# Optimization experiments

Hardware: AMD Instinct MI355X
Metric: run time of the kernel (lower is better)

The kernel has to match this reference:

```python
import jax, jax.numpy as jnp
import numpy as np

VOCAB = 50257
D = 768      # d_model
E = 4        # n_experts
R = 32       # low-rank expert rank
B = 4        # batch
T = 512      # seq_len
LN_EPS = 1e-5


def setup_inputs() -> dict:
    key = jax.random.key(0)
    ks = jax.random.split(key, 8)
    n = lambda k, shape, scale: jax.random.normal(k, shape, dtype=jnp.float32) * scale
    return {
        "idx": jax.random.randint(ks[0], (B, T), 0, VOCAB),
        "W_emb": n(ks[1], (VOCAB, D), 0.02),            # tied embedding / lm head
        "G": n(ks[2], (E, D), 0.02),                     # expert gating signatures
        "W_in": n(ks[3], (E, D, R), 1.0 / np.sqrt(D)),   # per-expert input proj
        "W_rec": n(ks[4], (E, R, R), 1.0 / np.sqrt(R)),  # per-expert recurrent matrix
        "W_out": n(ks[5], (E, R, D), 1.0 / np.sqrt(R)),  # per-expert output proj
        "ln_gamma": jnp.ones((D,), dtype=jnp.float32),
        "ln_beta": jnp.zeros((D,), dtype=jnp.float32),
    }


def _layernorm(x, g, b):
    m = jnp.mean(x, axis=-1, keepdims=True)
    v = jnp.var(x, axis=-1, keepdims=True)
    return (x - m) * jax.lax.rsqrt(v + LN_EPS) * g + b


def reference(idx, W_emb, G, W_in, W_rec, W_out, ln_gamma, ln_beta):
    # idx: [B,T] int64 token ids
    x = W_emb[idx]                      # [B,T,D] embedding gather
    xT = jnp.swapaxes(x, 0, 1)          # [T,B,D] scan over time
    nE, nR = W_in.shape[0], W_in.shape[2]
    s0 = jnp.zeros((nE, idx.shape[0], nR), dtype=x.dtype)  # reset_state at t=0

    def step(states, x_t):
        # states: [E,B,R] per-expert recurrent state; x_t: [B,D]
        scores = x_t @ G.T                                         # [B,E] routing
        onehot = jax.nn.one_hot(jnp.argmax(scores, axis=-1), nE,
                                dtype=x_t.dtype)                   # [B,E] winner
        cand = jnp.tanh(jnp.einsum('bd,edr->ebr', x_t, W_in)
                        + jnp.einsum('ebr,ers->ebs', states, W_rec))  # [E,B,R]
        sel = jnp.swapaxes(onehot, 0, 1)[..., None]                # [E,B,1]
        new_states = sel * cand + (1.0 - sel) * states             # winner updates state
        y = jnp.einsum('be,ebr,erd->bd', onehot, cand, W_out) + x_t  # residual out
        return new_states, y

    _, ys = jax.lax.scan(step, s0, xT)          # ys: [T,B,D]
    h = _layernorm(jnp.swapaxes(ys, 0, 1), ln_gamma, ln_beta)  # [B,T,D]
    logits = h @ W_emb.T                         # [B,T,VOCAB] tied head
    return logits
```

## Files before the change

### kernel.cpp

```cpp
#include <hip/hip_runtime.h>
#include <hip/hip_bf16.h>
#include <stdint.h>

#define VOCAB 50257
#define NPAD  50432
#define D 768
#define E 4
#define R 32
#define B 4
#define T 512
#define NTOK (B*T)

typedef float f32x4 __attribute__((ext_vector_type(4)));
typedef short s16x8 __attribute__((ext_vector_type(8)));

__device__ __forceinline__ void async16(const void* g, void* l) {
    __builtin_amdgcn_global_load_lds(
        (const __attribute__((address_space(1))) uint32_t*)g,
        (__attribute__((address_space(3))) uint32_t*)l, 16, 0, 0);
}

__global__ __launch_bounds__(256) void k_embed_route(
    const int* __restrict__ idx, const float* __restrict__ Wemb,
    const float* __restrict__ G, const float* __restrict__ Win,
    float* __restrict__ xbuf, int* __restrict__ winner, float* __restrict__ ubuf)
{
    int tok = blockIdx.x;
    int tid = threadIdx.x;
    __shared__ float xs[D];
    __shared__ float sc[E];
    __shared__ float up[8][R];

    int token = idx[tok];
    const float* wrow = Wemb + (size_t)token * D;
    float x0 = wrow[tid], x1 = wrow[tid + 256], x2 = wrow[tid + 512];
    xs[tid] = x0; xs[tid + 256] = x1; xs[tid + 512] = x2;
    float* xg = xbuf + (size_t)tok * D;
    xg[tid] = x0; xg[tid + 256] = x1; xg[tid + 512] = x2;
    __syncthreads();

    int wave = tid >> 6, lane = tid & 63;
    {
        const float* g = G + wave * D;
        float p = 0.f;
        for (int d = lane; d < D; d += 64) p += xs[d] * g[d];
        for (int off = 32; off; off >>= 1) p += __shfl_down(p, off);
        if (lane == 0) sc[wave] = p;
    }
    __syncthreads();
    float s0 = sc[0], s1 = sc[1], s2 = sc[2], s3 = sc[3];
    int e = 0; float best = s0;
    if (s1 > best) { best = s1; e = 1; }
    if (s2 > best) { best = s2; e = 2; }
    if (s3 > best) { best = s3; e = 3; }
    if (tid == 0) winner[tok] = e;

    int r = tid & 31, chunk = tid >> 5;
    const float* wi = Win + (size_t)e * D * R;
    float p = 0.f;
    int d0 = chunk * 96;
    for (int d = d0; d < d0 + 96; ++d) p += xs[d] * wi[d * R + r];
    up[chunk][r] = p;
    __syncthreads();
    if (tid < R) {
        float s = 0.f;
        #pragma unroll
        for (int ch = 0; ch < 8; ++ch) s += up[ch][tid];
        ubuf[(size_t)tok * R + tid] = s;
    }
}

__global__ __launch_bounds__(64) void k_scan(
    const int* __restrict__ winner, const float* __restrict__ ubuf,
    const float* __restrict__ Wrec, float* __restrict__ cbuf)
{
    int b = blockIdx.x >> 2;
    int e = blockIdx.x & 3;
    int j = threadIdx.x;
    __shared__ float s_lds[R];
    __shared__ int   tlist[T];

    const int* wb = winner + b * T;

    unsigned long long lanemask_lt = (j == 0) ? 0ull : (~0ull >> (64 - j));
    int base = 0;
    for (int rr = 0; rr < T / 64; ++rr) {
        int t = rr * 64 + j;
        bool match = (wb[t] == e);
        unsigned long long m = __ballot(match);
        if (match) tlist[base + __popcll(m & lanemask_lt)] = t;
        base += __popcll(m);
    }
    int total = base;

    float wr[R];
    if (j < R) {
        s_lds[j] = 0.f;
        #pragma unroll
        for (int i = 0; i < R; ++i) wr[i] = Wrec[(size_t)e * R * R + i * R + j];
    }
    __syncthreads();
    if (j >= R) return;

    const float* ub = ubuf + (size_t)b * T * R;
    float*       cb = cbuf + (size_t)b * T * R;

    int   t0 = 0, t1 = 0;
    float u0 = 0.f, u1 = 0.f;
    if (total > 0) { t0 = tlist[0]; u0 = ub[t0 * R + j]; }
    if (total > 1) { t1 = tlist[1]; u1 = ub[t1 * R + j]; }

    for (int k = 0; k < total; ++k) {
        int t = t0; float uj = u0;
        t0 = t1; u0 = u1;
        if (k + 2 < total) { int t2 = tlist[k + 2]; t1 = t2; u1 = ub[t2 * R + j]; }

        float a0 = uj, a1 = 0.f, a2 = 0.f, a3 = 0.f;
        #pragma unroll
        for (int q = 0; q < 8; ++q) {
            float4 sv = *(const float4*)&s_lds[q * 4];
            a0 += sv.x * wr[q * 4 + 0]; a1 += sv.y * wr[q * 4 + 1];
            a2 += sv.z * wr[q * 4 + 2]; a3 += sv.w * wr[q * 4 + 3];
        }
        float acc = (a0 + a1) + (a2 + a3);
        float ex = __expf(2.f * acc);
        float th = 1.f - 2.f * __builtin_amdgcn_rcpf(ex + 1.f);
        cb[t * R + j] = th;
        s_lds[j] = th;
    }
}

__global__ __launch_bounds__(256) void k_out_ln(
    const float* __restrict__ xbuf, const int* __restrict__ winner,
    const float* __restrict__ cbuf, const float* __restrict__ Wout,
    const float* __restrict__ gamma, const float* __restrict__ beta,
    __hip_bfloat16* __restrict__ hbuf)
{
    int tok = blockIdx.x, tid = threadIdx.x;
    __shared__ float cs[R];
    __shared__ float w1[4], w2[4];
    int e = winner[tok];
    if (tid < R) cs[tid] = cbuf[(size_t)tok * R + tid];
    __syncthreads();

    const float* wo = Wout + (size_t)e * R * D;
    const float* xg = xbuf + (size_t)tok * D;
    float y[3];
    #pragma unroll
    for (int kk = 0; kk < 3; ++kk) {
        int d = tid + kk * 256;
        float acc = xg[d];
        #pragma unroll
        for (int r = 0; r < R; ++r) acc += cs[r] * wo[r * D + d];
        y[kk] = acc;
    }
    float s1 = y[0] + y[1] + y[2];
    float s2 = y[0] * y[0] + y[1] * y[1] + y[2] * y[2];
    int wave = tid >> 6, lane = tid & 63;
    for (int off = 32; off; off >>= 1) { s1 += __shfl_down(s1, off); s2 += __shfl_down(s2, off); }
    if (lane == 0) { w1[wave] = s1; w2[wave] = s2; }
    __syncthreads();
    float m = (w1[0] + w1[1] + w1[2] + w1[3]) * (1.f / D);
    float v = (w2[0] + w2[1] + w2[2] + w2[3]) * (1.f / D) - m * m;
    float rstd = rsqrtf(v + 1e-5f);
    #pragma unroll
    for (int kk = 0; kk < 3; ++kk) {
        int d = tid + kk * 256;
        float hn = (y[kk] - m) * rstd * gamma[d] + beta[d];
        hbuf[(size_t)tok * D + d] = __float2bfloat16(hn);
    }
}

__global__ __launch_bounds__(256) void k_cvt(
    const float* __restrict__ Wemb, __hip_bfloat16* __restrict__ Wb)
{
    long i = (long)(blockIdx.x * 256 + threadIdx.x) * 4;
    const long total = (long)NPAD * D;
    const long valid = (long)VOCAB * D;
    if (i >= total) return;
    float4 v;
    if (i < valid) v = *(const float4*)(Wemb + i);
    else           v = make_float4(0.f, 0.f, 0.f, 0.f);
    union { ushort4 u4; __hip_bfloat16 h[4]; } pk;
    pk.h[0] = __float2bfloat16(v.x); pk.h[1] = __float2bfloat16(v.y);
    pk.h[2] = __float2bfloat16(v.z); pk.h[3] = __float2bfloat16(v.w);
    *(ushort4*)((unsigned short*)Wb + i) = pk.u4;
}

#define BM 256
#define BN 256
#define BK 64
#define MB (NTOK / BM)
#define NB (NPAD / BN)
#define NWG (MB * NB)
__global__ __launch_bounds__(512, 2) void k_gemm(
    const __hip_bfloat16* __restrict__ A,
    const __hip_bfloat16* __restrict__ Bm,
    float* __restrict__ Cmat)
{
    __shared__ __align__(16) char lds[131072];
    const int tid = threadIdx.x;
    const int orig = blockIdx.x;
    const int wg = (orig & 7) * (NWG / 8) + (orig >> 3);
    const int m0 = (wg & (MB - 1)) * BM;
    const int n0 = (wg / MB) * BN;
    const int wave = tid >> 6, lane = tid & 63;
    const int wm = (wave & 1) * 128;
    const int wn = (wave >> 1) * 64;
    const int l15 = lane & 15, quad = lane >> 4;

    f32x4 acc[8][4] = {};

    const int srowS = tid >> 2;
    const int skelS = (((tid & 3) ^ ((tid >> 2) & 3)) * 8);
    const size_t aBase = (size_t)(m0 + srowS) * 768 + skelS;
    const size_t bBase = (size_t)(n0 + srowS) * 768 + skelS;
    const int ldsPos = tid * 16;

    auto stageA = [&](char* buf, int kg, int h) {
        async16(A + aBase + kg + h * 32,                      buf + h * 16384 + ldsPos);
        async16(A + aBase + (size_t)128 * 768 + kg + h * 32,  buf + h * 16384 + 8192 + ldsPos);
    };
    auto stageB = [&](char* buf, int kg, int h) {
        async16(Bm + bBase + kg + h * 32,                     buf + 32768 + h * 16384 + ldsPos);
        async16(Bm + bBase + (size_t)128 * 768 + kg + h * 32, buf + 32768 + h * 16384 + 8192 + ldsPos);
    };

    const int swz = ((quad ^ (l15 & 3)) << 4);

    stageA(lds, 0, 0); stageB(lds, 0, 0); stageA(lds, 0, 1); stageB(lds, 0, 1);

    for (int t = 0; t < 12; ++t) {
        char* bufC = lds + (t & 1) * 65536;
        char* bufN = lds + ((t + 1) & 1) * 65536;
        const int k1 = (t + 1) * BK;
        const bool pre = (t < 11);
        s16x8 af[8], bfr[2];

        asm volatile("s_waitcnt vmcnt(4)" ::: "memory");
        __builtin_amdgcn_s_barrier();
        __builtin_amdgcn_sched_barrier(0);
        if (pre) stageA(bufN, k1, 0);
        #pragma unroll
        for (int i = 0; i < 8; ++i)
            af[i] = *(const s16x8*)(bufC + (wm + i * 16 + l15) * 64 + swz);
        #pragma unroll
        for (int j = 0; j < 2; ++j)
            bfr[j] = *(const s16x8*)(bufC + 32768 + (wn + j * 16 + l15) * 64 + swz);
        __builtin_amdgcn_s_setprio(1);
        #pragma unroll
        for (int i = 0; i < 8; ++i) {
            acc[i][0] = __builtin_amdgcn_mfma_f32_16x16x32_bf16(af[i], bfr[0], acc[i][0], 0, 0, 0);
            acc[i][1] = __builtin_amdgcn_mfma_f32_16x16x32_bf16(af[i], bfr[1], acc[i][1], 0, 0, 0);
        }
        __builtin_amdgcn_s_setprio(0);

        __builtin_amdgcn_s_barrier();
        __builtin_amdgcn_sched_barrier(0);
        if (pre) stageB(bufN, k1, 0);
        #pragma unroll
        for (int j = 0; j < 2; ++j)
            bfr[j] = *(const s16x8*)(bufC + 32768 + (wn + (j + 2) * 16 + l15) * 64 + swz);
        __builtin_amdgcn_s_setprio(1);
        #pragma unroll
        for (int i = 0; i < 8; ++i) {
            acc[i][2] = __builtin_amdgcn_mfma_f32_16x16x32_bf16(af[i], bfr[0], acc[i][2], 0, 0, 0);
            acc[i][3] = __builtin_amdgcn_mfma_f32_16x16x32_bf16(af[i], bfr[1], acc[i][3], 0, 0, 0);
        }
        __builtin_amdgcn_s_setprio(0);

        if (t == 11) asm volatile("s_waitcnt vmcnt(0)" ::: "memory");
        else         asm volatile("s_waitcnt vmcnt(4)" ::: "memory");
        __builtin_amdgcn_s_barrier();
        __builtin_amdgcn_sched_barrier(0);
        if (pre) stageA(bufN, k1, 1);
        #pragma unroll
        for (int i = 0; i < 8; ++i)
            af[i] = *(const s16x8*)(bufC + 16384 + (wm + i * 16 + l15) * 64 + swz);
        #pragma unroll
        for (int j = 0; j < 2; ++j)
            bfr[j] = *(const s16x8*)(bufC + 49152 + (wn + j * 16 + l15) * 64 + swz);
        __builtin_amdgcn_s_setprio(1);
        #pragma unroll
        for (int i = 0; i < 8; ++i) {
            acc[i][0] = __builtin_amdgcn_mfma_f32_16x16x32_bf16(af[i], bfr[0], acc[i][0], 0, 0, 0);
            acc[i][1] = __builtin_amdgcn_mfma_f32_16x16x32_bf16(af[i], bfr[1], acc[i][1], 0, 0, 0);
        }
        __builtin_amdgcn_s_setprio(0);

        __builtin_amdgcn_s_barrier();
        __builtin_amdgcn_sched_barrier(0);
        if (pre) stageB(bufN, k1, 1);
        #pragma unroll
        for (int j = 0; j < 2; ++j)
            bfr[j] = *(const s16x8*)(bufC + 49152 + (wn + (j + 2) * 16 + l15) * 64 + swz);
        __builtin_amdgcn_s_setprio(1);
        #pragma unroll
        for (int i = 0; i < 8; ++i) {
            acc[i][2] = __builtin_amdgcn_mfma_f32_16x16x32_bf16(af[i], bfr[0], acc[i][2], 0, 0, 0);
            acc[i][3] = __builtin_amdgcn_mfma_f32_16x16x32_bf16(af[i], bfr[1], acc[i][3], 0, 0, 0);
        }
        __builtin_amdgcn_s_setprio(0);
    }

    #pragma unroll
    for (int i = 0; i < 8; ++i) {
        #pragma unroll
        for (int j = 0; j < 4; ++j) {
            int col = n0 + wn + j * 16 + l15;
            if (col < VOCAB) {
                #pragma unroll
                for (int r = 0; r < 4; ++r) {
                    int row = m0 + wm + i * 16 + quad * 4 + r;
                    Cmat[(size_t)row * VOCAB + col] = acc[i][j][r];
                }
            }
        }
    }
}

extern "C" void kernel_launch(void* const* d_in, const int* in_sizes, int n_in,
                              void* d_out, int out_size, void* d_ws, size_t ws_size,
                              hipStream_t stream)
{
    const int*   idx   = (const int*)d_in[0];
    const float* Wemb  = (const float*)d_in[1];
    const float* G     = (const float*)d_in[2];
    const float* Win   = (const float*)d_in[3];
    const float* Wrec  = (const float*)d_in[4];
    const float* Wout  = (const float*)d_in[5];
    const float* gamma = (const float*)d_in[6];
    const float* beta  = (const float*)d_in[7];
    float* out = (float*)d_out;

    char* ws = (char*)d_ws;
    float*          xbuf   = (float*)(ws);
    int*            winner = (int*)  (ws + 6291456);
    float*          ubuf   = (float*)(ws + 6299648);
    float*          cbuf   = (float*)(ws + 6561792);
    __hip_bfloat16* hbuf   = (__hip_bfloat16*)(ws + 6823936);
    __hip_bfloat16* wembb  = (__hip_bfloat16*)(ws + 9969664);

    k_cvt<<<(NPAD * D / 4 + 255) / 256, 256, 0, stream>>>(Wemb, wembb);
    k_embed_route<<<NTOK, 256, 0, stream>>>(idx, Wemb, G, Win, xbuf, winner, ubuf);
    k_scan<<<B * E, 64, 0, stream>>>(winner, ubuf, Wrec, cbuf);
    k_out_ln<<<NTOK, 256, 0, stream>>>(xbuf, winner, cbuf, Wout, gamma, beta, hbuf);
    k_gemm<<<NWG, 512, 0, stream>>>(hbuf, wembb, out);
}
```

Before: 789.0 us.

## Fuse weight bf16 conversion into embed kernel and reorder GEMM LDS/barrier pipeline

The separate fp32-to-bf16 conversion kernel for the tied embedding is removed. Its grid-stride loop now runs inside k_embed_route, which saves a launch and lets the conversion overlap with the routing work. In the GEMM main loop, LDS fragment reads are now issued before the next async global-to-LDS stage and the barrier, with explicit lgkmcnt waits and sched_barriers. The aim is to overlap LDS reads with the barrier and prefetch issue. The new barrier placement has to keep the double buffer race-free, and the fused conversion loop adds long-running work to every embed block.

```diff
diff --git a/kernel.cpp b/kernel.cpp
--- a/kernel.cpp
+++ b/kernel.cpp
@@ -23,7 +23,8 @@
 __global__ __launch_bounds__(256) void k_embed_route(
     const int* __restrict__ idx, const float* __restrict__ Wemb,
     const float* __restrict__ G, const float* __restrict__ Win,
-    float* __restrict__ xbuf, int* __restrict__ winner, float* __restrict__ ubuf)
+    float* __restrict__ xbuf, int* __restrict__ winner, float* __restrict__ ubuf,
+    __hip_bfloat16* __restrict__ Wb)
 {
     int tok = blockIdx.x;
     int tid = threadIdx.x;
@@ -67,6 +68,18 @@
         #pragma unroll
         for (int ch = 0; ch < 8; ++ch) s += up[ch][tid];
         ubuf[(size_t)tok * R + tid] = s;
+    }
+
+    const long totalq = (long)NPAD * D / 4;
+    const long validq = (long)VOCAB * D / 4;
+    for (long i = (long)tok * 256 + tid; i < totalq; i += (long)NTOK * 256) {
+        float4 v;
+        if (i < validq) v = *(const float4*)(Wemb + i * 4);
+        else            v = make_float4(0.f, 0.f, 0.f, 0.f);
+        union { ushort4 u4; __hip_bfloat16 h[4]; } pk;
+        pk.h[0] = __float2bfloat16(v.x); pk.h[1] = __float2bfloat16(v.y);
+        pk.h[2] = __float2bfloat16(v.z); pk.h[3] = __float2bfloat16(v.w);
+        *(ushort4*)((unsigned short*)Wb + i * 4) = pk.u4;
     }
 }
 
@@ -171,28 +184,13 @@
     }
 }
 
-__global__ __launch_bounds__(256) void k_cvt(
-    const float* __restrict__ Wemb, __hip_bfloat16* __restrict__ Wb)
-{
-    long i = (long)(blockIdx.x * 256 + threadIdx.x) * 4;
-    const long total = (long)NPAD * D;
-    const long valid = (long)VOCAB * D;
-    if (i >= total) return;
-    float4 v;
-    if (i < valid) v = *(const float4*)(Wemb + i);
-    else           v = make_float4(0.f, 0.f, 0.f, 0.f);
-    union { ushort4 u4; __hip_bfloat16 h[4]; } pk;
-    pk.h[0] = __float2bfloat16(v.x); pk.h[1] = __float2bfloat16(v.y);
-    pk.h[2] = __float2bfloat16(v.z); pk.h[3] = __float2bfloat16(v.w);
-    *(ushort4*)((unsigned short*)Wb + i) = pk.u4;
-}
-
 #define BM 256
 #define BN 256
 #define BK 64
 #define MB (NTOK / BM)
 #define NB (NPAD / BN)
 #define NWG (MB * NB)
+#define SB __builtin_amdgcn_sched_barrier(0)
 __global__ __launch_bounds__(512, 2) void k_gemm(
     const __hip_bfloat16* __restrict__ A,
     const __hip_bfloat16* __restrict__ Bm,
@@ -229,6 +227,8 @@
     const int swz = ((quad ^ (l15 & 3)) << 4);
 
     stageA(lds, 0, 0); stageB(lds, 0, 0); stageA(lds, 0, 1); stageB(lds, 0, 1);
+    asm volatile("s_waitcnt vmcnt(4)" ::: "memory");
+    __builtin_amdgcn_s_barrier();
 
     for (int t = 0; t < 12; ++t) {
         char* bufC = lds + (t & 1) * 65536;
@@ -237,70 +237,75 @@
         const bool pre = (t < 11);
         s16x8 af[8], bfr[2];
 
-        asm volatile("s_waitcnt vmcnt(4)" ::: "memory");
-        __builtin_amdgcn_s_barrier();
-        __builtin_amdgcn_sched_barrier(0);
-        if (pre) stageA(bufN, k1, 0);
         #pragma unroll
         for (int i = 0; i < 8; ++i)
             af[i] = *(const s16x8*)(bufC + (wm + i * 16 + l15) * 64 + swz);
         #pragma unroll
         for (int j = 0; j < 2; ++j)
             bfr[j] = *(const s16x8*)(bufC + 32768 + (wn + j * 16 + l15) * 64 + swz);
+        if (pre) stageA(bufN, k1, 0);
+        SB; __builtin_amdgcn_s_barrier();
+        asm volatile("s_waitcnt lgkmcnt(0)" ::: "memory"); SB;
         __builtin_amdgcn_s_setprio(1);
         #pragma unroll
         for (int i = 0; i < 8; ++i) {
             acc[i][0] = __builtin_amdgcn_mfma_f32_16x16x32_bf16(af[i], bfr[0], acc[i][0], 0, 0, 0);
             acc[i][1] = __builtin_amdgcn_mfma_f32_16x16x32_bf16(af[i], bfr[1], acc[i][1], 0, 0, 0);
         }
-        __builtin_amdgcn_s_setprio(0);
-
+        __builtin_amdgcn_s_setprio(0); SB;
         __builtin_amdgcn_s_barrier();
-        __builtin_amdgcn_sched_barrier(0);
-        if (pre) stageB(bufN, k1, 0);
+
         #pragma unroll
         for (int j = 0; j < 2; ++j)
             bfr[j] = *(const s16x8*)(bufC + 32768 + (wn + (j + 2) * 16 + l15) * 64 + swz);
+        if (pre) stageB(bufN, k1, 0);
+        SB; __builtin_amdgcn_s_barrier();
+        asm volatile("s_waitcnt lgkmcnt(0)" ::: "memory"); SB;
         __builtin_amdgcn_s_setprio(1);
         #pragma unroll
         for (int i = 0; i < 8; ++i) {
             acc[i][2] = __builtin_amdgcn_mfma_f32_16x16x32_bf16(af[i], bfr[0], acc[i][2], 0, 0, 0);
             acc[i][3] = __builtin_amdgcn_mfma_f32_16x16x32_bf16(af[i], bfr[1], acc[i][3], 0, 0, 0);
         }
-        __builtin_amdgcn_s_setprio(0);
-
-        if (t == 11) asm volatile("s_waitcnt vmcnt(0)" ::: "memory");
-        else         asm volatile("s_waitcnt vmcnt(4)" ::: "memory");
+        __builtin_amdgcn_s_setprio(0); SB;
+        if (pre) asm volatile("s_waitcnt vmcnt(4)" ::: "memory");
+        else     asm volatile("s_waitcnt vmcnt(0)" ::: "memory");
         __builtin_amdgcn_s_barrier();
-        __builtin_amdgcn_sched_barrier(0);
-        if (pre) stageA(bufN, k1, 1);
+
         #pragma unroll
         for (int i = 0; i < 8; ++i)
             af[i] = *(const s16x8*)(bufC + 16384 + (wm + i * 16 + l15) * 64 + swz);
         #pragma unroll
         for (int j = 0; j < 2; ++j)
             bfr[j] = *(const s16x8*)(bufC + 49152 + (wn + j * 16 + l15) * 64 + swz);
+        if (pre) stageA(bufN, k1, 1);
+        SB; __builtin_amdgcn_s_barrier();
+        asm volatile("s_waitcnt lgkmcnt(0)" ::: "memory"); SB;
         __builtin_amdgcn_s_setprio(1);
         #pragma unroll
         for (int i = 0; i < 8; ++i) {
             acc[i][0] = __builtin_amdgcn_mfma_f32_16x16x32_bf16(af[i], bfr[0], acc[i][0], 0, 0, 0);
             acc[i][1] = __builtin_amdgcn_mfma_f32_16x16x32_bf16(af[i], bfr[1], acc[i][1], 0, 0, 0);
         }
-        __builtin_amdgcn_s_setprio(0);
-
+        __builtin_amdgcn_s_setprio(0); SB;
         __builtin_amdgcn_s_barrier();
-        __builtin_amdgcn_sched_barrier(0);
-        if (pre) stageB(bufN, k1, 1);
+
         #pragma unroll
         for (int j = 0; j < 2; ++j)
             bfr[j] = *(const s16x8*)(bufC + 49152 + (wn + (j + 2) * 16 + l15) * 64 + swz);
+        if (pre) stageB(bufN, k1, 1);
+        SB; __builtin_amdgcn_s_barrier();
+        asm volatile("s_waitcnt lgkmcnt(0)" ::: "memory"); SB;
         __builtin_amdgcn_s_setprio(1);
         #pragma unroll
         for (int i = 0; i < 8; ++i) {
             acc[i][2] = __builtin_amdgcn_mfma_f32_16x16x32_bf16(af[i], bfr[0], acc[i][2], 0, 0, 0);
             acc[i][3] = __builtin_amdgcn_mfma_f32_16x16x32_bf16(af[i], bfr[1], acc[i][3], 0, 0, 0);
         }
-        __builtin_amdgcn_s_setprio(0);
+        __builtin_amdgcn_s_setprio(0); SB;
+        if (pre) asm volatile("s_waitcnt vmcnt(4)" ::: "memory");
+        else     asm volatile("s_waitcnt vmcnt(0)" ::: "memory");
+        __builtin_amdgcn_s_barrier();
     }
 
     #pragma unroll
@@ -341,8 +346,7 @@
     __hip_bfloat16* hbuf   = (__hip_bfloat16*)(ws + 6823936);
     __hip_bfloat16* wembb  = (__hip_bfloat16*)(ws + 9969664);
 
-    k_cvt<<<(NPAD * D / 4 + 255) / 256, 256, 0, stream>>>(Wemb, wembb);
-    k_embed_route<<<NTOK, 256, 0, stream>>>(idx, Wemb, G, Win, xbuf, winner, ubuf);
+    k_embed_route<<<NTOK, 256, 0, stream>>>(idx, Wemb, G, Win, xbuf, winner, ubuf, wembb);
     k_scan<<<B * E, 64, 0, stream>>>(winner, ubuf, Wrec, cbuf);
     k_out_ln<<<NTOK, 256, 0, stream>>>(xbuf, winner, cbuf, Wout, gamma, beta, hbuf);
     k_gemm<<<NWG, 512, 0, stream>>>(hbuf, wembb, out);
```

New measurement: 806.6 us. 2.2% more time.
